# Optimization experiments

Measured on AMD Instinct MI355X. Metric: run time of the kernel, lower is better.

## Reference

```python
import jax, jax.numpy as jnp
import numpy as np

B, D, UNITS = 512, 256, 256

def setup_inputs() -> dict:
    key = jax.random.key(0)
    k1, k2, k3, k4 = jax.random.split(key, 4)
    mu_in = jax.random.normal(k1, (B, D), dtype=jnp.float32)
    Sigma_in = jax.random.normal(k2, (B, D, D), dtype=jnp.float32) * 0.01
    # w_mu ~ N(0, 0.05); w_sigma ~ U(-4.5, -2.2) per build()
    w_mu = 0.05 * jax.random.normal(k3, (D, UNITS), dtype=jnp.float32)
    w_sigma = jax.random.uniform(k4, (UNITS,), dtype=jnp.float32, minval=-4.5, maxval=-2.2)
    return {"mu_in": mu_in, "Sigma_in": Sigma_in, "w_mu": w_mu, "w_sigma": w_sigma}


def reference(mu_in, Sigma_in, w_mu, w_sigma):
    # mu_out = mu_in @ w_mu                         [B, units]
    mu_out = jnp.matmul(mu_in, w_mu)
    units = w_sigma.shape[0]
    sp = jax.nn.softplus(w_sigma)                   # softplus(w_sigma), [units]
    W_Sigma = jnp.diag(sp)                          # [units, units]
    # Sigma_1 = w_mu^T @ Sigma_in @ w_mu            [B, units, units]
    Sigma_1 = jnp.einsum('du,bde,ev->buv', w_mu, Sigma_in, w_mu)
    # Sigma_2 = (x.x^T scalar) * W_Sigma            [B, units, units]
    xx_t = jnp.sum(mu_in * mu_in, axis=1)           # [B]
    Sigma_2 = xx_t[:, None, None] * W_Sigma
    # Sigma_3 = trace(Sigma_in) * W_Sigma           [B, units, units]
    tr = jnp.trace(Sigma_in, axis1=1, axis2=2)      # [B]
    Sigma_3 = tr[:, None, None] * W_Sigma
    Sigma_out = Sigma_1 + Sigma_2 + Sigma_3
    # NaN/Inf cleanup -> zeros (matches two tf.where calls)
    Sigma_out = jnp.where(jnp.isfinite(Sigma_out), Sigma_out, jnp.zeros_like(Sigma_out))
    # set_diag(Sigma_out, |diag(Sigma_out)|)
    eye = jnp.eye(units, dtype=bool)
    Sigma_out = jnp.where(eye, jnp.abs(Sigma_out), Sigma_out)
    return (mu_out, Sigma_out)
```

## Files before the change

kernel.cpp:

```cpp
#include <hip/hip_runtime.h>

#define BATCH 512
#define DIM   256
#define UNITS 256

typedef __bf16 bf16x8 __attribute__((ext_vector_type(8)));
typedef float  f32x4  __attribute__((ext_vector_type(4)));

__device__ __forceinline__ bf16x8 ld_bf8(const unsigned short* p) {
    uint4 u = *reinterpret_cast<const uint4*>(p);
    return __builtin_bit_cast(bf16x8, u);
}

__device__ __forceinline__ unsigned short bfc(float f) {
    return __builtin_bit_cast(unsigned short, (__bf16)f);
}

__device__ __forceinline__ bf16x8 cvt8(float4 a, float4 b) {
    bf16x8 r;
    r[0] = (__bf16)a.x; r[1] = (__bf16)a.y; r[2] = (__bf16)a.z; r[3] = (__bf16)a.w;
    r[4] = (__bf16)b.x; r[5] = (__bf16)b.y; r[6] = (__bf16)b.z; r[7] = (__bf16)b.w;
    return r;
}

__device__ __forceinline__ void gload16(void* lds, const void* g) {
    __builtin_amdgcn_global_load_lds(
        (const __attribute__((address_space(1))) unsigned int*)g,
        (__attribute__((address_space(3))) unsigned int*)lds, 16, 0, 0);
}

__global__ __launch_bounds__(256) void prep_kernel(
    const float* __restrict__ mu_in, const float* __restrict__ Sigma,
    const float* __restrict__ W, const float* __restrict__ w_sigma,
    float* __restrict__ mu_out, unsigned short* __restrict__ Wt2,
    float* __restrict__ sb, float* __restrict__ sp)
{
    const int b = blockIdx.x;
    const int t = threadIdx.x;

    __shared__ float mrow[DIM];
    mrow[t] = mu_in[b * DIM + t];
    __syncthreads();

    float acc = 0.f;
#pragma unroll 8
    for (int d = 0; d < DIM; ++d) acc += mrow[d] * W[d * UNITS + t];
    mu_out[b * UNITS + t] = acc;

    float xv  = mrow[t];
    float val = xv * xv + Sigma[(size_t)b * DIM * DIM + (size_t)t * (DIM + 1)];
#pragma unroll
    for (int o = 32; o > 0; o >>= 1) val += __shfl_down(val, o);
    __shared__ float wsum[4];
    if ((t & 63) == 0) wsum[t >> 6] = val;
    __syncthreads();
    if (t == 0) sb[b] = wsum[0] + wsum[1] + wsum[2] + wsum[3];

    if (b < UNITS) {
        const int u   = b;
        const int idx = ((u >> 4) * 8 + (t >> 5)) * 512 + ((t >> 3) & 3) * 128
                      + (u & 15) * 8 + (t & 7);
        Wt2[idx] = bfc(W[t * UNITS + u]);
    }
    if (b == 0) sp[t] = log1pf(expf(w_sigma[t]));
}

__global__ __launch_bounds__(512, 4) void sigma_kernel(
    const float* __restrict__ Sigma, const unsigned short* __restrict__ Wt2,
    const float* __restrict__ sb, const float* __restrict__ sp,
    float* __restrict__ out)
{
    __shared__ __align__(1024) char smem[128 * 264 * 2];
    auto Pt = reinterpret_cast<unsigned short (*)[264]>(smem);

    const int bid     = blockIdx.x;
    const int logical = (bid & 7) * 128 + (bid >> 3);
    const int b       = logical >> 1;
    const int h       = logical & 1;
    const int v0      = h * 128;
    const int s8      = h * 8;

    const int tid  = threadIdx.x;
    const int lane = tid & 63;
    const int w    = tid >> 6;
    const int lq   = lane >> 4;
    const int lr   = lane & 15;
    const int m0   = w * 32;

    const float* S = Sigma + (size_t)b * DIM * DIM;
    float*       O = out   + (size_t)b * UNITS * UNITS;
    const float  sbv = sb[b];

    const int rsub = lane >> 3;
    const int csrc = (lane & 7) ^ rsub;
    const char* gbase = (const char*)S + (size_t)(w * 32 + rsub) * 1024 + csrc * 16;
    const int   ldsw  = w * 4096;

    const int h7 = lr & 7;
    const int a0r = (m0 + lr) * 128;
    const int a1r = (m0 + 16 + lr) * 128;
    const int c0  = ((2 * lq + 0) ^ h7) * 16;
    const int c1  = ((2 * lq + 1) ^ h7) * 16;

    f32x4 acc[2][8];
#pragma unroll
    for (int i = 0; i < 2; ++i)
#pragma unroll
        for (int j = 0; j < 8; ++j)
#pragma unroll
            for (int r = 0; r < 4; ++r) acc[i][j][r] = 0.f;

#pragma unroll
    for (int q = 0; q < 4; ++q)
        gload16(smem + ldsw + q * 1024, gbase + q * 8192);
    __syncthreads();

#pragma unroll
    for (int kk = 0; kk < 8; ++kk) {
        const int cur = (kk & 1) * 32768;
        if (kk < 7) {
            const int nxt = cur ^ 32768;
#pragma unroll
            for (int q = 0; q < 4; ++q)
                gload16(smem + nxt + ldsw + q * 1024,
                        gbase + q * 8192 + (kk + 1) * 128);
        }
        float4 fa0 = *reinterpret_cast<const float4*>(smem + cur + a0r + c0);
        float4 fb0 = *reinterpret_cast<const float4*>(smem + cur + a0r + c1);
        float4 fa1 = *reinterpret_cast<const float4*>(smem + cur + a1r + c0);
        float4 fb1 = *reinterpret_cast<const float4*>(smem + cur + a1r + c1);
        bf16x8 af0 = cvt8(fa0, fb0);
        bf16x8 af1 = cvt8(fa1, fb1);
#pragma unroll
        for (int j = 0; j < 8; ++j) {
            bf16x8 bf = ld_bf8(Wt2 + (size_t)((s8 + j) * 8 + kk) * 512 + lane * 8);
            acc[0][j] = __builtin_amdgcn_mfma_f32_16x16x32_bf16(af0, bf, acc[0][j], 0, 0, 0);
            acc[1][j] = __builtin_amdgcn_mfma_f32_16x16x32_bf16(af1, bf, acc[1][j], 0, 0, 0);
        }
        __syncthreads();
    }

#pragma unroll
    for (int i = 0; i < 2; ++i) {
#pragma unroll
        for (int j = 0; j < 8; ++j) {
            const int d0 = m0 + 16 * i + 4 * lq;
            const int vl = 16 * j + lr;
            uint2 pk;
            pk.x = (unsigned)bfc(acc[i][j][0]) | ((unsigned)bfc(acc[i][j][1]) << 16);
            pk.y = (unsigned)bfc(acc[i][j][2]) | ((unsigned)bfc(acc[i][j][3]) << 16);
            *reinterpret_cast<uint2*>(&Pt[vl][d0]) = pk;
        }
    }
    __syncthreads();

#pragma unroll
    for (int i = 0; i < 2; ++i)
#pragma unroll
        for (int j = 0; j < 8; ++j)
#pragma unroll
            for (int r = 0; r < 4; ++r) acc[i][j][r] = 0.f;

#pragma unroll
    for (int kk = 0; kk < 8; ++kk) {
        bf16x8 af0 = ld_bf8(Wt2 + (size_t)((w * 2 + 0) * 8 + kk) * 512 + lane * 8);
        bf16x8 af1 = ld_bf8(Wt2 + (size_t)((w * 2 + 1) * 8 + kk) * 512 + lane * 8);
#pragma unroll
        for (int j = 0; j < 8; ++j) {
            bf16x8 pb = *reinterpret_cast<const bf16x8*>(&Pt[16 * j + lr][kk * 32 + 8 * lq]);
            acc[0][j] = __builtin_amdgcn_mfma_f32_16x16x32_bf16(af0, pb, acc[0][j], 0, 0, 0);
            acc[1][j] = __builtin_amdgcn_mfma_f32_16x16x32_bf16(af1, pb, acc[1][j], 0, 0, 0);
        }
    }

#pragma unroll
    for (int i = 0; i < 2; ++i) {
#pragma unroll
        for (int j = 0; j < 8; ++j) {
            const int   vg  = v0 + 16 * j + lr;
            const float spv = sp[vg];
#pragma unroll
            for (int r = 0; r < 4; ++r) {
                const int u = m0 + 16 * i + 4 * lq + r;
                float val = acc[i][j][r];
                if (u == vg) val += sbv * spv;
                val = __builtin_isfinite(val) ? val : 0.0f;
                if (u == vg) val = fabsf(val);
                O[(size_t)u * UNITS + vg] = val;
            }
        }
    }
}

extern "C" void kernel_launch(void* const* d_in, const int* in_sizes, int n_in,
                              void* d_out, int out_size, void* d_ws, size_t ws_size,
                              hipStream_t stream) {
    const float* mu_in  = (const float*)d_in[0];
    const float* Sigma  = (const float*)d_in[1];
    const float* w_mu   = (const float*)d_in[2];
    const float* w_sig  = (const float*)d_in[3];

    float* mu_out  = (float*)d_out;
    float* Sig_out = (float*)d_out + BATCH * UNITS;

    unsigned short* Wt2 = (unsigned short*)d_ws;
    float* sb = (float*)((char*)d_ws + (size_t)DIM * UNITS * 2);
    float* sp = sb + BATCH;

    prep_kernel<<<BATCH, 256, 0, stream>>>(mu_in, Sigma, w_mu, w_sig, mu_out, Wt2, sb, sp);
    sigma_kernel<<<BATCH * 2, 512, 0, stream>>>(Sigma, Wt2, sb, sp, Sig_out);
}
```

Baseline: 87.26 us.

## Use one 1024-thread block per batch with LDS-staged W and fine-grained waits

Replaces the two half-column blocks per batch with a single 1024-thread block that computes the full 256x256 output. This removes the redundant recomputation of Sigma@W that each half-block did before. W fragments are now staged into a 4-deep LDS ring via global_load_lds, using explicit vmcnt waits and raw barriers instead of __syncthreads. The intermediate is stored in a swizzled 256x256 bf16 LDS tile. The cost is 128KB of LDS per block and larger blocks, which reduces occupancy to one block per CU and makes the manual waitcnt accounting fragile.

```diff
diff --git a/kernel.cpp b/kernel.cpp
--- a/kernel.cpp
+++ b/kernel.cpp
@@ -6,6 +6,8 @@
 
 typedef __bf16 bf16x8 __attribute__((ext_vector_type(8)));
 typedef float  f32x4  __attribute__((ext_vector_type(4)));
+
+#define VMWAIT(N) asm volatile("s_waitcnt vmcnt(" #N ")" ::: "memory")
 
 __device__ __forceinline__ bf16x8 ld_bf8(const unsigned short* p) {
     uint4 u = *reinterpret_cast<const uint4*>(p);
@@ -65,129 +67,122 @@
     if (b == 0) sp[t] = log1pf(expf(w_sigma[t]));
 }
 
-__global__ __launch_bounds__(512, 4) void sigma_kernel(
+__global__ __launch_bounds__(1024, 4) void sigma_kernel(
     const float* __restrict__ Sigma, const unsigned short* __restrict__ Wt2,
     const float* __restrict__ sb, const float* __restrict__ sp,
     float* __restrict__ out)
 {
-    __shared__ __align__(1024) char smem[128 * 264 * 2];
-    auto Pt = reinterpret_cast<unsigned short (*)[264]>(smem);
-
-    const int bid     = blockIdx.x;
-    const int logical = (bid & 7) * 128 + (bid >> 3);
-    const int b       = logical >> 1;
-    const int h       = logical & 1;
-    const int v0      = h * 128;
-    const int s8      = h * 8;
-
+    __shared__ __align__(1024) char smem[131072];
+    char* slab = smem + 65536;
+
+    const int b    = blockIdx.x;
     const int tid  = threadIdx.x;
     const int lane = tid & 63;
     const int w    = tid >> 6;
     const int lq   = lane >> 4;
     const int lr   = lane & 15;
-    const int m0   = w * 32;
 
     const float* S = Sigma + (size_t)b * DIM * DIM;
     float*       O = out   + (size_t)b * UNITS * UNITS;
     const float  sbv = sb[b];
 
-    const int rsub = lane >> 3;
-    const int csrc = (lane & 7) ^ rsub;
-    const char* gbase = (const char*)S + (size_t)(w * 32 + rsub) * 1024 + csrc * 16;
-    const int   ldsw  = w * 4096;
-
-    const int h7 = lr & 7;
-    const int a0r = (m0 + lr) * 128;
-    const int a1r = (m0 + 16 + lr) * 128;
-    const int c0  = ((2 * lq + 0) ^ h7) * 16;
-    const int c1  = ((2 * lq + 1) ^ h7) * 16;
-
-    f32x4 acc[2][8];
-#pragma unroll
-    for (int i = 0; i < 2; ++i)
-#pragma unroll
-        for (int j = 0; j < 8; ++j)
-#pragma unroll
-            for (int r = 0; r < 4; ++r) acc[i][j][r] = 0.f;
-
-#pragma unroll
-    for (int q = 0; q < 4; ++q)
-        gload16(smem + ldsw + q * 1024, gbase + q * 8192);
-    __syncthreads();
+    const int srw  = lane >> 3;
+    const int csrc = ((lane & 7) ^ srw) * 16;
+    const char* gS0 = (const char*)S + (size_t)(16 * w + srw) * 1024 + csrc;
+    const char* gS1 = gS0 + 8 * 1024;
+
+    const unsigned short* wfrag = Wt2 + (size_t)w * 8 * 512 + lane * 8;
+
+    const int arow = (16 * w + lr) * 128;
+    const int h7   = lr & 7;
+    const int c0   = ((2 * lq + 0) ^ h7) * 16;
+    const int c1   = ((2 * lq + 1) ^ h7) * 16;
+
+    f32x4 acc[16];
+#pragma unroll
+    for (int j = 0; j < 16; ++j)
+#pragma unroll
+        for (int r = 0; r < 4; ++r) acc[j][r] = 0.f;
+
+    gload16(slab + 0 * 16384 + w * 1024, wfrag + 0 * 512);
+    gload16(smem + 0 * 32768 + (2 * w + 0) * 1024, gS0);
+    gload16(smem + 0 * 32768 + (2 * w + 1) * 1024, gS1);
+    gload16(slab + 1 * 16384 + w * 1024, wfrag + 1 * 512);
 
 #pragma unroll
     for (int kk = 0; kk < 8; ++kk) {
-        const int cur = (kk & 1) * 32768;
         if (kk < 7) {
-            const int nxt = cur ^ 32768;
-#pragma unroll
-            for (int q = 0; q < 4; ++q)
-                gload16(smem + nxt + ldsw + q * 1024,
-                        gbase + q * 8192 + (kk + 1) * 128);
-        }
-        float4 fa0 = *reinterpret_cast<const float4*>(smem + cur + a0r + c0);
-        float4 fb0 = *reinterpret_cast<const float4*>(smem + cur + a0r + c1);
-        float4 fa1 = *reinterpret_cast<const float4*>(smem + cur + a1r + c0);
-        float4 fb1 = *reinterpret_cast<const float4*>(smem + cur + a1r + c1);
-        bf16x8 af0 = cvt8(fa0, fb0);
-        bf16x8 af1 = cvt8(fa1, fb1);
-#pragma unroll
-        for (int j = 0; j < 8; ++j) {
-            bf16x8 bf = ld_bf8(Wt2 + (size_t)((s8 + j) * 8 + kk) * 512 + lane * 8);
-            acc[0][j] = __builtin_amdgcn_mfma_f32_16x16x32_bf16(af0, bf, acc[0][j], 0, 0, 0);
-            acc[1][j] = __builtin_amdgcn_mfma_f32_16x16x32_bf16(af1, bf, acc[1][j], 0, 0, 0);
-        }
-        __syncthreads();
-    }
-
-#pragma unroll
-    for (int i = 0; i < 2; ++i) {
-#pragma unroll
-        for (int j = 0; j < 8; ++j) {
-            const int d0 = m0 + 16 * i + 4 * lq;
-            const int vl = 16 * j + lr;
+            char* d = smem + ((kk + 1) & 1) * 32768;
+            gload16(d + (2 * w + 0) * 1024, gS0 + (kk + 1) * 128);
+            gload16(d + (2 * w + 1) * 1024, gS1 + (kk + 1) * 128);
+        }
+        if (kk < 6)
+            gload16(slab + ((kk + 2) & 3) * 16384 + w * 1024,
+                    wfrag + (kk + 2) * 512);
+
+        if (kk < 6)       { VMWAIT(4); }
+        else if (kk == 6) { VMWAIT(3); }
+        else              { VMWAIT(0); }
+        __builtin_amdgcn_s_barrier();
+
+        const char* sc = smem + (kk & 1) * 32768;
+        float4 fa0 = *reinterpret_cast<const float4*>(sc + arow + c0);
+        float4 fa1 = *reinterpret_cast<const float4*>(sc + arow + c1);
+        bf16x8 af  = cvt8(fa0, fa1);
+
+        const char* sl = slab + (kk & 3) * 16384;
+#pragma unroll
+        for (int j = 0; j < 16; ++j) {
+            bf16x8 pb = *reinterpret_cast<const bf16x8*>(sl + j * 1024 + lane * 16);
+            acc[j] = __builtin_amdgcn_mfma_f32_16x16x32_bf16(af, pb, acc[j], 0, 0, 0);
+        }
+    }
+
+    __syncthreads();
+
+    {
+        const int chb = 2 * w + (lq >> 1);
+        const int sub = 8 * (lq & 1);
+#pragma unroll
+        for (int j = 0; j < 16; ++j) {
+            const int v = 16 * j + lr;
             uint2 pk;
-            pk.x = (unsigned)bfc(acc[i][j][0]) | ((unsigned)bfc(acc[i][j][1]) << 16);
-            pk.y = (unsigned)bfc(acc[i][j][2]) | ((unsigned)bfc(acc[i][j][3]) << 16);
-            *reinterpret_cast<uint2*>(&Pt[vl][d0]) = pk;
-        }
-    }
-    __syncthreads();
-
-#pragma unroll
-    for (int i = 0; i < 2; ++i)
-#pragma unroll
-        for (int j = 0; j < 8; ++j)
-#pragma unroll
-            for (int r = 0; r < 4; ++r) acc[i][j][r] = 0.f;
+            pk.x = (unsigned)bfc(acc[j][0]) | ((unsigned)bfc(acc[j][1]) << 16);
+            pk.y = (unsigned)bfc(acc[j][2]) | ((unsigned)bfc(acc[j][3]) << 16);
+            *reinterpret_cast<uint2*>(smem + v * 512 + ((chb ^ (v & 7)) * 16) + sub) = pk;
+        }
+    }
+    __syncthreads();
+
+#pragma unroll
+    for (int j = 0; j < 16; ++j)
+#pragma unroll
+        for (int r = 0; r < 4; ++r) acc[j][r] = 0.f;
 
 #pragma unroll
     for (int kk = 0; kk < 8; ++kk) {
-        bf16x8 af0 = ld_bf8(Wt2 + (size_t)((w * 2 + 0) * 8 + kk) * 512 + lane * 8);
-        bf16x8 af1 = ld_bf8(Wt2 + (size_t)((w * 2 + 1) * 8 + kk) * 512 + lane * 8);
-#pragma unroll
-        for (int j = 0; j < 8; ++j) {
-            bf16x8 pb = *reinterpret_cast<const bf16x8*>(&Pt[16 * j + lr][kk * 32 + 8 * lq]);
-            acc[0][j] = __builtin_amdgcn_mfma_f32_16x16x32_bf16(af0, pb, acc[0][j], 0, 0, 0);
-            acc[1][j] = __builtin_amdgcn_mfma_f32_16x16x32_bf16(af1, pb, acc[1][j], 0, 0, 0);
-        }
-    }
-
-#pragma unroll
-    for (int i = 0; i < 2; ++i) {
-#pragma unroll
-        for (int j = 0; j < 8; ++j) {
-            const int   vg  = v0 + 16 * j + lr;
-            const float spv = sp[vg];
-#pragma unroll
-            for (int r = 0; r < 4; ++r) {
-                const int u = m0 + 16 * i + 4 * lq + r;
-                float val = acc[i][j][r];
-                if (u == vg) val += sbv * spv;
-                val = __builtin_isfinite(val) ? val : 0.0f;
-                if (u == vg) val = fabsf(val);
-                O[(size_t)u * UNITS + vg] = val;
-            }
+        bf16x8 af = ld_bf8(wfrag + kk * 512);
+#pragma unroll
+        for (int j = 0; j < 16; ++j) {
+            const int v  = 16 * j + lr;
+            const int ch = (4 * kk + lq) ^ (v & 7);
+            bf16x8 pb = *reinterpret_cast<const bf16x8*>(smem + v * 512 + ch * 16);
+            acc[j] = __builtin_amdgcn_mfma_f32_16x16x32_bf16(af, pb, acc[j], 0, 0, 0);
+        }
+    }
+
+#pragma unroll
+    for (int j = 0; j < 16; ++j) {
+        const int   vg  = 16 * j + lr;
+        const float spv = sp[vg];
+#pragma unroll
+        for (int r = 0; r < 4; ++r) {
+            const int u = 16 * w + 4 * lq + r;
+            float val = acc[j][r];
+            if (u == vg) val += sbv * spv;
+            val = __builtin_isfinite(val) ? val : 0.0f;
+            if (u == vg) val = fabsf(val);
+            O[(size_t)u * UNITS + vg] = val;
         }
     }
 }
@@ -208,5 +203,5 @@
     float* sp = sb + BATCH;
 
     prep_kernel<<<BATCH, 256, 0, stream>>>(mu_in, Sigma, w_mu, w_sig, mu_out, Wt2, sb, sp);
-    sigma_kernel<<<BATCH * 2, 512, 0, stream>>>(Sigma, Wt2, sb, sp, Sig_out);
-}
+    sigma_kernel<<<BATCH, 1024, 0, stream>>>(Sigma, Wt2, sb, sp, Sig_out);
+}
```

New measurement: 97.76 us. +12.0%, slower.
